# Performance work log

Hardware: AMD Instinct MI355X
Metric: run time of the kernel (lower is better)

The kernel has to match this reference:

```python
import jax, jax.numpy as jnp
import numpy as np

EPS = 1e-12  # matches torch.nn.functional.normalize eps


def setup_inputs() -> dict:
    key = jax.random.key(0)
    inputs = jax.random.normal(key, (128, 64, 64, 32), dtype=jnp.float32)
    return {"inputs": inputs}


def reference(inputs) -> jnp.ndarray:
    B, N = inputs.shape[0], inputs.shape[1]
    x = inputs.reshape(B, N, -1)                       # (B, N, D)
    norm = jnp.linalg.norm(x, axis=2, keepdims=True)   # (B, N, 1)
    att = x / jnp.maximum(norm, EPS)                   # L2-normalized rows
    # full N x N self-similarity per batch element
    sim = jnp.einsum('bnd,bmd->bnm', att, att)         # (B, N, N)
    diag_mean = (att * att).sum(axis=2).sum(axis=1).mean()
    loss = sim.sum(axis=(1, 2)).mean() - diag_mean
    return loss
```

## Files before the change

kernel.cpp:

```cpp
#include <hip/hip_runtime.h>
#include <math.h>

#define BB 128
#define NN 64
#define DD 2048
#define NBLK1 512
#define MAGIC 0x5A5A5A5Au

typedef float f4 __attribute__((ext_vector_type(4)));

__device__ __forceinline__ float wave_reduce_sum_down(float v) {
    #pragma unroll
    for (int off = 32; off > 0; off >>= 1)
        v += __shfl_down(v, off, 64);
    return v;
}

__device__ __forceinline__ void store_coherent(f4* p, f4 v) {
    asm volatile("global_store_dwordx4 %0, %1, off sc0 sc1 nt"
                 :: "v"(p), "v"(v) : "memory");
}

__global__ __launch_bounds__(256) void fused_kernel(
        const float* __restrict__ x,
        float* __restrict__ vseg,
        double* __restrict__ diag_seg,
        unsigned* __restrict__ flags,
        double* __restrict__ partials,
        unsigned* __restrict__ pflags,
        float* __restrict__ out) {
    const int u = blockIdx.x;
    const int b = u >> 2, s = u & 3;
    const int t = threadIdx.x;
    const int lane = t & 63, w = t >> 6;

    const float* xw = x + ((size_t)b * NN + s * 16 + w * 4) * DD;

    f4 a[4][8];
    #pragma unroll
    for (int r = 0; r < 4; ++r) {
        const f4* p = reinterpret_cast<const f4*>(xw + (size_t)r * DD);
        #pragma unroll
        for (int j = 0; j < 8; ++j)
            a[r][j] = __builtin_nontemporal_load(&p[lane + 64 * j]);
    }

    float ss[4];
    #pragma unroll
    for (int r = 0; r < 4; ++r) {
        float s4 = 0.f;
        #pragma unroll
        for (int j = 0; j < 8; ++j)
            s4 += a[r][j].x * a[r][j].x + a[r][j].y * a[r][j].y
                + a[r][j].z * a[r][j].z + a[r][j].w * a[r][j].w;
        ss[r] = s4;
    }

    #pragma unroll
    for (int off = 1; off < 64; off <<= 1) {
        float s0 = __shfl_xor(ss[0], off, 64);
        float s1 = __shfl_xor(ss[1], off, 64);
        float s2 = __shfl_xor(ss[2], off, 64);
        float s3 = __shfl_xor(ss[3], off, 64);
        ss[0] += s0; ss[1] += s1; ss[2] += s2; ss[3] += s3;
    }

    f4 acc[8];
    #pragma unroll
    for (int j = 0; j < 8; ++j) acc[j] = (f4)(0.f);
    float diag = 0.f;
    #pragma unroll
    for (int r = 0; r < 4; ++r) {
        const float inv = 1.0f / fmaxf(sqrtf(ss[r]), 1e-12f);
        diag += ss[r] * inv * inv;
        #pragma unroll
        for (int j = 0; j < 8; ++j) {
            acc[j].x = fmaf(a[r][j].x, inv, acc[j].x);
            acc[j].y = fmaf(a[r][j].y, inv, acc[j].y);
            acc[j].z = fmaf(a[r][j].z, inv, acc[j].z);
            acc[j].w = fmaf(a[r][j].w, inv, acc[j].w);
        }
    }

    __shared__ float lds[4][DD];
    __shared__ float dl[4];
    __shared__ float red[4];
    f4* lw = reinterpret_cast<f4*>(lds[w]);
    #pragma unroll
    for (int j = 0; j < 8; ++j) lw[lane + 64 * j] = acc[j];
    if (lane == 0) dl[w] = diag;
    __syncthreads();

    f4 o0 = (f4)(0.f), o1 = (f4)(0.f);
    #pragma unroll
    for (int ww = 0; ww < 4; ++ww) {
        const f4* lr = reinterpret_cast<const f4*>(lds[ww]);
        o0 += lr[t];
        o1 += lr[t + 256];
    }
    const double dsum = (double)dl[0] + dl[1] + dl[2] + dl[3];

    if (s != 3) {
        f4* dst = reinterpret_cast<f4*>(vseg + (size_t)u * DD);
        store_coherent(&dst[t], o0);
        store_coherent(&dst[t + 256], o1);
        if (t == 0)
            __hip_atomic_store(&diag_seg[u], dsum,
                               __ATOMIC_RELAXED, __HIP_MEMORY_SCOPE_AGENT);
        asm volatile("s_waitcnt vmcnt(0)" ::: "memory");
        __syncthreads();
        if (t == 0)
            __hip_atomic_store(&flags[u], MAGIC,
                               __ATOMIC_RELAXED, __HIP_MEMORY_SCOPE_AGENT);
        return;
    }

    if (t < 3) {
        const unsigned* f = &flags[(u & ~3) + t];
        while (__hip_atomic_load(f, __ATOMIC_RELAXED,
                                 __HIP_MEMORY_SCOPE_AGENT) != MAGIC) {}
    }
    __syncthreads();

    {
        const f4* s0p = reinterpret_cast<const f4*>(vseg + (size_t)(b * 4 + 0) * DD);
        const f4* s1p = reinterpret_cast<const f4*>(vseg + (size_t)(b * 4 + 1) * DD);
        const f4* s2p = reinterpret_cast<const f4*>(vseg + (size_t)(b * 4 + 2) * DD);
        f4 r0, r1, r2, r3, r4, r5;
        asm volatile(
            "global_load_dwordx4 %0, %6, off sc0 sc1\n\t"
            "global_load_dwordx4 %1, %7, off sc0 sc1\n\t"
            "global_load_dwordx4 %2, %8, off sc0 sc1\n\t"
            "global_load_dwordx4 %3, %9, off sc0 sc1\n\t"
            "global_load_dwordx4 %4, %10, off sc0 sc1\n\t"
            "global_load_dwordx4 %5, %11, off sc0 sc1\n\t"
            "s_waitcnt vmcnt(0)"
            : "=&v"(r0), "=&v"(r1), "=&v"(r2),
              "=&v"(r3), "=&v"(r4), "=&v"(r5)
            : "v"(&s0p[t]), "v"(&s1p[t]), "v"(&s2p[t]),
              "v"(&s0p[t + 256]), "v"(&s1p[t + 256]), "v"(&s2p[t + 256])
            : "memory");
        f4 c0 = r0 + r1 + r2 + o0;
        f4 c1 = r3 + r4 + r5 + o1;
        float p = c0.x * c0.x + c0.y * c0.y + c0.z * c0.z + c0.w * c0.w
                + c1.x * c1.x + c1.y * c1.y + c1.z * c1.z + c1.w * c1.w;
        p = wave_reduce_sum_down(p);
        if (lane == 0) red[w] = p;
    }
    __syncthreads();
    if (t == 0) {
        double sp = (double)red[0] + (double)red[1]
                  + (double)red[2] + (double)red[3];
        double dp = dsum;
        #pragma unroll
        for (int o = 0; o < 3; ++o)
            dp += __hip_atomic_load(&diag_seg[b * 4 + o],
                        __ATOMIC_RELAXED, __HIP_MEMORY_SCOPE_AGENT);
        __hip_atomic_store(&partials[b], sp - dp,
                           __ATOMIC_RELAXED, __HIP_MEMORY_SCOPE_AGENT);
        asm volatile("s_waitcnt vmcnt(0)" ::: "memory");
        __hip_atomic_store(&pflags[b], MAGIC,
                           __ATOMIC_RELAXED, __HIP_MEMORY_SCOPE_AGENT);
    }
    if (u != NBLK1 - 1) return;

    __syncthreads();
    if (t < BB - 1) {
        const unsigned* f = &pflags[t];
        while (__hip_atomic_load(f, __ATOMIC_RELAXED,
                                 __HIP_MEMORY_SCOPE_AGENT) != MAGIC) {}
    }
    __syncthreads();

    __shared__ double sd[BB];
    if (t < BB)
        sd[t] = __hip_atomic_load(&partials[t],
                        __ATOMIC_RELAXED, __HIP_MEMORY_SCOPE_AGENT);
    __syncthreads();
    #pragma unroll
    for (int off = BB / 2; off > 0; off >>= 1) {
        if (t < off) sd[t] += sd[t + off];
        __syncthreads();
    }
    if (t == 0) out[0] = (float)(sd[0] / (double)BB);
}

extern "C" void kernel_launch(void* const* d_in, const int* in_sizes, int n_in,
                              void* d_out, int out_size, void* d_ws, size_t ws_size,
                              hipStream_t stream) {
    const float* x = (const float*)d_in[0];
    float* out = (float*)d_out;
    char* ws = (char*)d_ws;

    const size_t vbytes = (size_t)NBLK1 * DD * 4;
    float* vseg       = (float*)ws;
    double* diag_seg  = (double*)(ws + vbytes);
    unsigned* flags   = (unsigned*)(ws + vbytes + 4096);
    double* partials  = (double*)(ws + vbytes + 4096 + 2048);
    unsigned* pflags  = (unsigned*)(ws + vbytes + 4096 + 2048 + 1024);

    fused_kernel<<<NBLK1, 256, 0, stream>>>(x, vseg, diag_seg, flags,
                                            partials, pflags, out);
}
```

Before: 18.19 us.

## Split each batch across two 512-thread blocks instead of four 256-thread blocks

Changes the decomposition so each batch element is handled by two blocks of eight waves (32 rows each) instead of four blocks of four waves. This halves the number of cross-block partial vectors written to and re-read from global memory, and reduces the flag-spin dependency to a single producer per consumer. In exchange there are half as many blocks (256) on the device, each using twice the LDS, which may lower parallelism and memory-level concurrency for the load phase.

```diff
diff --git a/kernel.cpp b/kernel.cpp
--- a/kernel.cpp
+++ b/kernel.cpp
@@ -4,7 +4,8 @@
 #define BB 128
 #define NN 64
 #define DD 2048
-#define NBLK1 512
+#define NBLK 256
+#define NTHR 512
 #define MAGIC 0x5A5A5A5Au
 
 typedef float f4 __attribute__((ext_vector_type(4)));
@@ -21,7 +22,7 @@
                  :: "v"(p), "v"(v) : "memory");
 }
 
-__global__ __launch_bounds__(256) void fused_kernel(
+__global__ __launch_bounds__(NTHR, 2) void fused_kernel(
         const float* __restrict__ x,
         float* __restrict__ vseg,
         double* __restrict__ diag_seg,
@@ -30,11 +31,11 @@
         unsigned* __restrict__ pflags,
         float* __restrict__ out) {
     const int u = blockIdx.x;
-    const int b = u >> 2, s = u & 3;
+    const int b = u >> 1, s = u & 1;
     const int t = threadIdx.x;
     const int lane = t & 63, w = t >> 6;
 
-    const float* xw = x + ((size_t)b * NN + s * 16 + w * 4) * DD;
+    const float* xw = x + ((size_t)b * NN + s * 32 + w * 4) * DD;
 
     f4 a[4][8];
     #pragma unroll
@@ -82,28 +83,26 @@
         }
     }
 
-    __shared__ float lds[4][DD];
-    __shared__ float dl[4];
-    __shared__ float red[4];
+    __shared__ float lds[8][DD];
+    __shared__ float dl[8];
+    __shared__ float red[8];
     f4* lw = reinterpret_cast<f4*>(lds[w]);
     #pragma unroll
     for (int j = 0; j < 8; ++j) lw[lane + 64 * j] = acc[j];
     if (lane == 0) dl[w] = diag;
     __syncthreads();
 
-    f4 o0 = (f4)(0.f), o1 = (f4)(0.f);
+    f4 o = (f4)(0.f);
     #pragma unroll
-    for (int ww = 0; ww < 4; ++ww) {
-        const f4* lr = reinterpret_cast<const f4*>(lds[ww]);
-        o0 += lr[t];
-        o1 += lr[t + 256];
-    }
-    const double dsum = (double)dl[0] + dl[1] + dl[2] + dl[3];
+    for (int ww = 0; ww < 8; ++ww)
+        o += reinterpret_cast<const f4*>(lds[ww])[t];
+    double dsum = 0.0;
+    #pragma unroll
+    for (int ww = 0; ww < 8; ++ww) dsum += (double)dl[ww];
 
-    if (s != 3) {
+    if (s == 0) {
         f4* dst = reinterpret_cast<f4*>(vseg + (size_t)u * DD);
-        store_coherent(&dst[t], o0);
-        store_coherent(&dst[t + 256], o1);
+        store_coherent(&dst[t], o);
         if (t == 0)
             __hip_atomic_store(&diag_seg[u], dsum,
                                __ATOMIC_RELAXED, __HIP_MEMORY_SCOPE_AGENT);
@@ -115,54 +114,42 @@
         return;
     }
 
-    if (t < 3) {
-        const unsigned* f = &flags[(u & ~3) + t];
+    if (t == 0) {
+        const unsigned* f = &flags[u - 1];
         while (__hip_atomic_load(f, __ATOMIC_RELAXED,
                                  __HIP_MEMORY_SCOPE_AGENT) != MAGIC) {}
     }
     __syncthreads();
 
     {
-        const f4* s0p = reinterpret_cast<const f4*>(vseg + (size_t)(b * 4 + 0) * DD);
-        const f4* s1p = reinterpret_cast<const f4*>(vseg + (size_t)(b * 4 + 1) * DD);
-        const f4* s2p = reinterpret_cast<const f4*>(vseg + (size_t)(b * 4 + 2) * DD);
-        f4 r0, r1, r2, r3, r4, r5;
+        const f4* sp = reinterpret_cast<const f4*>(vseg + (size_t)(u - 1) * DD);
+        f4 r0;
         asm volatile(
-            "global_load_dwordx4 %0, %6, off sc0 sc1\n\t"
-            "global_load_dwordx4 %1, %7, off sc0 sc1\n\t"
-            "global_load_dwordx4 %2, %8, off sc0 sc1\n\t"
-            "global_load_dwordx4 %3, %9, off sc0 sc1\n\t"
-            "global_load_dwordx4 %4, %10, off sc0 sc1\n\t"
-            "global_load_dwordx4 %5, %11, off sc0 sc1\n\t"
+            "global_load_dwordx4 %0, %1, off sc0 sc1\n\t"
             "s_waitcnt vmcnt(0)"
-            : "=&v"(r0), "=&v"(r1), "=&v"(r2),
-              "=&v"(r3), "=&v"(r4), "=&v"(r5)
-            : "v"(&s0p[t]), "v"(&s1p[t]), "v"(&s2p[t]),
-              "v"(&s0p[t + 256]), "v"(&s1p[t + 256]), "v"(&s2p[t + 256])
+            : "=&v"(r0)
+            : "v"(&sp[t])
             : "memory");
-        f4 c0 = r0 + r1 + r2 + o0;
-        f4 c1 = r3 + r4 + r5 + o1;
-        float p = c0.x * c0.x + c0.y * c0.y + c0.z * c0.z + c0.w * c0.w
-                + c1.x * c1.x + c1.y * c1.y + c1.z * c1.z + c1.w * c1.w;
+        f4 c = r0 + o;
+        float p = c.x * c.x + c.y * c.y + c.z * c.z + c.w * c.w;
         p = wave_reduce_sum_down(p);
         if (lane == 0) red[w] = p;
     }
     __syncthreads();
     if (t == 0) {
-        double sp = (double)red[0] + (double)red[1]
-                  + (double)red[2] + (double)red[3];
-        double dp = dsum;
+        double sp2 = 0.0;
         #pragma unroll
-        for (int o = 0; o < 3; ++o)
-            dp += __hip_atomic_load(&diag_seg[b * 4 + o],
+        for (int ww = 0; ww < 8; ++ww) sp2 += (double)red[ww];
+        double dp = dsum
+                  + __hip_atomic_load(&diag_seg[u - 1],
                         __ATOMIC_RELAXED, __HIP_MEMORY_SCOPE_AGENT);
-        __hip_atomic_store(&partials[b], sp - dp,
+        __hip_atomic_store(&partials[b], sp2 - dp,
                            __ATOMIC_RELAXED, __HIP_MEMORY_SCOPE_AGENT);
         asm volatile("s_waitcnt vmcnt(0)" ::: "memory");
         __hip_atomic_store(&pflags[b], MAGIC,
                            __ATOMIC_RELAXED, __HIP_MEMORY_SCOPE_AGENT);
     }
-    if (u != NBLK1 - 1) return;
+    if (u != NBLK - 1) return;
 
     __syncthreads();
     if (t < BB - 1) {
@@ -192,13 +179,13 @@
     float* out = (float*)d_out;
     char* ws = (char*)d_ws;
 
-    const size_t vbytes = (size_t)NBLK1 * DD * 4;
+    const size_t vbytes = (size_t)NBLK * DD * 4;
     float* vseg       = (float*)ws;
     double* diag_seg  = (double*)(ws + vbytes);
-    unsigned* flags   = (unsigned*)(ws + vbytes + 4096);
-    double* partials  = (double*)(ws + vbytes + 4096 + 2048);
-    unsigned* pflags  = (unsigned*)(ws + vbytes + 4096 + 2048 + 1024);
+    unsigned* flags   = (unsigned*)(ws + vbytes + 2048);
+    double* partials  = (double*)(ws + vbytes + 2048 + 1024);
+    unsigned* pflags  = (unsigned*)(ws + vbytes + 2048 + 1024 + 1024);
 
-    fused_kernel<<<NBLK1, 256, 0, stream>>>(x, vseg, diag_seg, flags,
+    fused_kernel<<<NBLK, NTHR, 0, stream>>>(x, vseg, diag_seg, flags,
                                             partials, pflags, out);
 }
```

Result: slower. 20.06 us (+10.3%).
